# Kernel optimization log

Measured on AMD Instinct MI355X. Metric: run time of the kernel, lower is better.

Reference implementation:

```python
import jax, jax.numpy as jnp
import numpy as np

B, N_PER, F_IN, H1, EMB, N_ACT = 8, 50000, 64, 128, 64, 64
E_PER = 50000
N = B * N_PER  # flat node count


def setup_inputs() -> dict:
    key = jax.random.key(0)
    ks = jax.random.split(key, 6)
    s = lambda d: 1.0 / np.sqrt(d)
    return {
        "node_features": jax.random.normal(ks[0], (B, N_PER, F_IN), jnp.float32),
        "edge_index": jax.random.randint(ks[1], (B, 2, E_PER), 0, N, jnp.int64),
        "W1": jax.random.normal(ks[2], (F_IN, H1), jnp.float32) * s(F_IN),
        "b1": jnp.zeros((H1,), jnp.float32),
        "W2": jax.random.normal(ks[3], (H1, EMB), jnp.float32) * s(H1),
        "b2": jnp.zeros((EMB,), jnp.float32),
        "fc_w": jax.random.normal(ks[4], (EMB, EMB), jnp.float32) * s(EMB),
        "fc_b": jnp.zeros((EMB,), jnp.float32),
        "out_w": jax.random.normal(ks[5], (EMB, N_ACT), jnp.float32) * s(EMB),
        "out_b": jnp.zeros((N_ACT,), jnp.float32),
    }


def _gcn_conv(x, W, b, src, dst, n):
    # PyG GCNConv: add self-loops, symmetric deg normalization, then
    # out_i = sum_{j->i} norm_ji * (x_j @ W) + b
    loop = jnp.arange(n, dtype=src.dtype)
    s2 = jnp.concatenate([src, loop])
    d2 = jnp.concatenate([dst, loop])
    deg = jax.ops.segment_sum(jnp.ones_like(s2, dtype=x.dtype), d2, num_segments=n)
    dis = jnp.where(deg > 0, jax.lax.rsqrt(deg), 0.0)
    norm = dis[s2] * dis[d2]  # [E+N]
    h = x @ W  # [n, out]
    msg = h[s2] * norm[:, None]  # gather + scale
    return jax.ops.segment_sum(msg, d2, num_segments=n) + b


def reference(node_features, edge_index, W1, b1, W2, b2, fc_w, fc_b, out_w, out_b):
    b_, n_, f_ = node_features.shape
    x = node_features.reshape(-1, f_)  # [B*N, F]
    ei = edge_index.reshape(2, -1)     # matches torch .view(2, -1) on contiguous tensor
    src, dst = ei[0], ei[1]
    n = b_ * n_
    x = jax.nn.relu(_gcn_conv(x, W1, b1, src, dst, n))
    x = jax.nn.relu(_gcn_conv(x, W2, b2, src, dst, n))
    # global_mean_pool with batch = arange(B).repeat_interleave(N): nodes are contiguous
    pooled = x.reshape(b_, n_, -1).mean(axis=1)  # [B, EMB]
    h = jax.nn.relu(pooled @ fc_w + fc_b)
    return h @ out_w + out_b  # [B, num_actions]
```

## Files before the change

kernel.cpp:

```cpp
#include <hip/hip_runtime.h>

#define NPER 50000
#define NB 8
#define FIN 64
#define NH1 128
#define NEMB 64

typedef __attribute__((ext_vector_type(8))) short short8;
typedef __attribute__((ext_vector_type(4))) float f32x4;
union U4S8 { uint4 q; short8 s; };

__device__ inline float bf2f(unsigned int u){ union{unsigned int i; float f;} v; v.i = u<<16; return v.f; }
__device__ inline unsigned int f2bf1(float f){ union{float f; unsigned int i;} v; v.f = f;
  return (v.i + 0x7FFFu + ((v.i>>16)&1u)) >> 16; }
__device__ inline unsigned int packbf(float lo, float hi){ return f2bf1(lo) | (f2bf1(hi)<<16); }
__device__ inline void unp8add(float* s, uint4 q){
  s[0]+=bf2f(q.x&0xFFFFu); s[1]+=bf2f(q.x>>16);
  s[2]+=bf2f(q.y&0xFFFFu); s[3]+=bf2f(q.y>>16);
  s[4]+=bf2f(q.z&0xFFFFu); s[5]+=bf2f(q.z>>16);
  s[6]+=bf2f(q.w&0xFFFFu); s[7]+=bf2f(q.w>>16);
}

__global__ void k_detect(const int* __restrict__ ei, int* __restrict__ flag){
  __shared__ int any;
  if(threadIdx.x == 0) any = 0;
  __syncthreads();
  for(int i = threadIdx.x; i < 2048; i += 256){
    if(ei[2*i + 1] != 0) any = 1;
  }
  __syncthreads();
  if(threadIdx.x == 0) *flag = (any == 0) ? 1 : 0;
}
__device__ inline int load_edge(const int* __restrict__ ei, int idx, bool is64){
  return is64 ? ei[2*idx] : ei[idx];
}

__global__ void k_packW(const float* __restrict__ W1, const float* __restrict__ W2,
                        unsigned int* __restrict__ w1p, unsigned int* __restrict__ w2p){
  int tid = threadIdx.x;
  for(int s = tid; s < 1024; s += 256){
    int f = s >> 6, lane = s & 63;
    int nt = f >> 1, kb = f & 1, g = lane >> 4, c = nt*16 + (lane & 15);
    unsigned int o[4];
    #pragma unroll
    for(int j = 0; j < 4; j++){
      int k0 = kb*32 + g*8 + 2*j;
      o[j] = packbf(W1[k0*NH1 + c], W1[(k0+1)*NH1 + c]);
    }
    *(uint4*)(w1p + s*4) = make_uint4(o[0],o[1],o[2],o[3]);
  }
  for(int s = tid; s < 1024; s += 256){
    int f = s >> 6, lane = s & 63;
    int nt = f >> 2, kb = f & 3, g = lane >> 4, c = nt*16 + (lane & 15);
    unsigned int o[4];
    #pragma unroll
    for(int j = 0; j < 4; j++){
      int k0 = kb*32 + g*8 + 2*j;
      o[j] = packbf(W2[k0*NEMB + c], W2[(k0+1)*NEMB + c]);
    }
    *(uint4*)(w2p + s*4) = make_uint4(o[0],o[1],o[2],o[3]);
  }
}

__global__ void k_count(const int* __restrict__ ei, const int* __restrict__ flag,
                        int* __restrict__ ideg, int E){
  int e = blockIdx.x*256 + threadIdx.x;
  if(e < E){
    bool is64 = (*flag != 0);
    int d = load_edge(ei, E + e, is64);
    atomicAdd(&ideg[d], 1);
  }
}

__global__ void k_scan1(const int* __restrict__ ideg, int* __restrict__ bsum, int n){
  __shared__ int red[256];
  int i0 = blockIdx.x*1024 + threadIdx.x*4;
  int t = 0;
  #pragma unroll
  for(int j = 0; j < 4; j++) if(i0+j < n) t += ideg[i0+j];
  red[threadIdx.x] = t;
  __syncthreads();
  for(int off = 128; off > 0; off >>= 1){
    if(threadIdx.x < off) red[threadIdx.x] += red[threadIdx.x + off];
    __syncthreads();
  }
  if(threadIdx.x == 0) bsum[blockIdx.x] = red[0];
}

__global__ void k_scan2(int* __restrict__ bsum, int* __restrict__ row_start, int nblk, int n){
  __shared__ int sm[512];
  int t = threadIdx.x;
  int v = (t < nblk) ? bsum[t] : 0;
  sm[t] = v;
  __syncthreads();
  for(int off = 1; off < 512; off <<= 1){
    int a = (t >= off) ? sm[t - off] : 0;
    __syncthreads();
    sm[t] += a;
    __syncthreads();
  }
  if(t < nblk) bsum[t] = sm[t] - v;
  if(t == 511) row_start[n] = sm[511];
}

__global__ void k_scan3(const int* __restrict__ ideg, const int* __restrict__ bsum,
                        int* __restrict__ row_start, int* __restrict__ cursor, int n){
  __shared__ int red[256];
  int i0 = blockIdx.x*1024 + threadIdx.x*4;
  int v[4]; int t = 0;
  #pragma unroll
  for(int j = 0; j < 4; j++){ v[j] = (i0+j < n) ? ideg[i0+j] : 0; t += v[j]; }
  red[threadIdx.x] = t;
  __syncthreads();
  for(int off = 1; off < 256; off <<= 1){
    int a = (threadIdx.x >= off) ? red[threadIdx.x - off] : 0;
    __syncthreads();
    red[threadIdx.x] += a;
    __syncthreads();
  }
  int run = bsum[blockIdx.x] + red[threadIdx.x] - t;
  #pragma unroll
  for(int j = 0; j < 4; j++){
    if(i0+j < n){ row_start[i0+j] = run; cursor[i0+j] = run; run += v[j]; }
  }
}

__global__ void k_dis(const int* __restrict__ ideg, float* __restrict__ dis, int n){
  int i = blockIdx.x*256 + threadIdx.x;
  if(i < n) dis[i] = rsqrtf((float)ideg[i] + 1.0f);
}

__global__ void k_fill(const int* __restrict__ ei, const int* __restrict__ flag,
                       int* __restrict__ cursor, int* __restrict__ src_list, int E){
  int e = blockIdx.x*256 + threadIdx.x;
  if(e < E){
    bool is64 = (*flag != 0);
    int s = load_edge(ei, e, is64);
    int d = load_edge(ei, E + e, is64);
    int pos = atomicAdd(&cursor[d], 1);
    src_list[pos] = s;
  }
}

__global__ __launch_bounds__(256) void k_gemm1m(const float* __restrict__ x, const unsigned int* __restrict__ w1p,
                                                const float* __restrict__ dis, unsigned int* __restrict__ g1, int n){
  __shared__ unsigned short tile[4][2176];
  const int tid = threadIdx.x;
  const int wm = tid >> 6, lane = tid & 63;
  const int m16 = lane & 15, g = lane >> 4;
  const int base = blockIdx.x*64;
  const int nodeA = base + wm*16 + m16;
  short8 a[2];
  #pragma unroll
  for(int kb = 0; kb < 2; kb++){
    float4 v0, v1;
    if(nodeA < n){
      const float* xp = x + (size_t)nodeA*FIN + kb*32 + g*8;
      v0 = *(const float4*)xp; v1 = *(const float4*)(xp + 4);
    } else { v0 = make_float4(0,0,0,0); v1 = v0; }
    U4S8 u;
    u.q.x = packbf(v0.x, v0.y); u.q.y = packbf(v0.z, v0.w);
    u.q.z = packbf(v1.x, v1.y); u.q.w = packbf(v1.z, v1.w);
    a[kb] = u.s;
  }
  f32x4 acc[8] = {};
  #pragma unroll
  for(int nt = 0; nt < 8; nt++){
    #pragma unroll
    for(int kb = 0; kb < 2; kb++){
      U4S8 b; b.q = *(const uint4*)(w1p + ((nt*2 + kb)*64 + lane)*4);
      acc[nt] = __builtin_amdgcn_mfma_f32_16x16x32_bf16(a[kb], b.s, acc[nt], 0, 0, 0);
    }
  }
  float dr[4];
  #pragma unroll
  for(int i = 0; i < 4; i++){ int r = base + wm*16 + 4*g + i; dr[i] = (r < n) ? dis[r] : 0.f; }
  unsigned short* T = tile[wm];
  #pragma unroll
  for(int nt = 0; nt < 8; nt++)
    #pragma unroll
    for(int i = 0; i < 4; i++)
      T[(4*g + i)*136 + nt*16 + m16] = (unsigned short)f2bf1(acc[nt][i] * dr[i]);
  __syncthreads();
  int r = lane >> 2;
  int node2 = base + wm*16 + r;
  if(node2 < n){
    uint4* dst = (uint4*)(g1 + (size_t)node2*64);
    #pragma unroll
    for(int j = 0; j < 4; j++){
      int q = (lane & 3)*4 + j;
      dst[q] = *(const uint4*)(T + r*136 + q*8);
    }
  }
}

__global__ __launch_bounds__(256) void k_fused1m(const unsigned int* __restrict__ g1, const unsigned int* __restrict__ w2p,
                                                 const float* __restrict__ dis, const float* __restrict__ b1,
                                                 const int* __restrict__ row_start, const int* __restrict__ src_list,
                                                 unsigned int* __restrict__ g2, int n){
  __shared__ unsigned int x1T[4352];
  const int tid = threadIdx.x;
  const int base = blockIdx.x*64;
  {
    int nl = tid >> 2, qc = tid & 3;
    int node = base + nl;
    int rbase = nl*68 + qc*16;
    int sw = (nl & 7) << 2;
    if(node < n){
      float s[32];
      #pragma unroll
      for(int j = 0; j < 32; j++) s[j] = 0.f;
      const uint4* self = (const uint4*)(g1 + (size_t)node*64 + qc*16);
      { uint4 q0 = self[0], q1 = self[1], q2 = self[2], q3 = self[3];
        unp8add(s, q0); unp8add(s+8, q1); unp8add(s+16, q2); unp8add(s+24, q3); }
      int r0 = row_start[node], r1 = row_start[node+1];
      for(int e = r0; e < r1; e++){
        const uint4* p = (const uint4*)(g1 + (size_t)src_list[e]*64 + qc*16);
        uint4 q0 = p[0], q1 = p[1], q2 = p[2], q3 = p[3];
        unp8add(s, q0); unp8add(s+8, q1); unp8add(s+16, q2); unp8add(s+24, q3);
      }
      float d = dis[node];
      const float* bb = b1 + qc*32;
      unsigned int ob[16];
      #pragma unroll
      for(int j = 0; j < 16; j++){
        float v0 = fmaxf(fmaf(d, s[2*j],   bb[2*j]),   0.f);
        float v1 = fmaxf(fmaf(d, s[2*j+1], bb[2*j+1]), 0.f);
        ob[j] = packbf(v0, v1);
      }
      #pragma unroll
      for(int j = 0; j < 4; j++)
        *(uint4*)(x1T + ((rbase + j*4) ^ sw)) = make_uint4(ob[4*j], ob[4*j+1], ob[4*j+2], ob[4*j+3]);
    } else {
      #pragma unroll
      for(int j = 0; j < 4; j++)
        *(uint4*)(x1T + ((rbase + j*4) ^ sw)) = make_uint4(0,0,0,0);
    }
  }
  __syncthreads();
  const int wm = tid >> 6, lane = tid & 63, m16 = lane & 15, g = lane >> 4;
  const int row = wm*16 + m16;
  const int swr = (row & 7) << 2;
  f32x4 acc[4] = {};
  #pragma unroll
  for(int kb = 0; kb < 4; kb++){
    U4S8 a; a.q = *(const uint4*)(x1T + ((row*68 + kb*16 + g*4) ^ swr));
    #pragma unroll
    for(int nt = 0; nt < 4; nt++){
      U4S8 b; b.q = *(const uint4*)(w2p + ((nt*4 + kb)*64 + lane)*4);
      acc[nt] = __builtin_amdgcn_mfma_f32_16x16x32_bf16(a.s, b.s, acc[nt], 0, 0, 0);
    }
  }
  __syncthreads();
  unsigned short* T = (unsigned short*)x1T + wm*1152;
  float dr[4];
  #pragma unroll
  for(int i = 0; i < 4; i++){ int r = base + wm*16 + 4*g + i; dr[i] = (r < n) ? dis[r] : 0.f; }
  #pragma unroll
  for(int nt = 0; nt < 4; nt++)
    #pragma unroll
    for(int i = 0; i < 4; i++)
      T[(4*g + i)*72 + nt*16 + m16] = (unsigned short)f2bf1(acc[nt][i] * dr[i]);
  __syncthreads();
  int r = lane >> 2;
  int node2 = base + wm*16 + r;
  if(node2 < n){
    uint4* dst = (uint4*)(g2 + (size_t)node2*32);
    #pragma unroll
    for(int j = 0; j < 2; j++){
      int q = ((lane & 3) << 1) + j;
      dst[q] = *(const uint4*)(T + r*72 + q*8);
    }
  }
}

__global__ __launch_bounds__(256) void k_fused2p(const unsigned int* __restrict__ g2,
                                                 const float* __restrict__ dis, const float* __restrict__ b2,
                                                 const int* __restrict__ row_start, const int* __restrict__ src_list,
                                                 float* __restrict__ pooled, int n){
  __shared__ float red[256*17];
  const int tid = threadIdx.x;
  const int base = blockIdx.x*64;
  int nl = tid >> 2, qc = tid & 3;
  int node = base + nl;
  float s[16];
  #pragma unroll
  for(int j = 0; j < 16; j++) s[j] = 0.f;
  if(node < n){
    const uint4* self = (const uint4*)(g2 + (size_t)node*32 + qc*8);
    { uint4 q0 = self[0], q1 = self[1]; unp8add(s, q0); unp8add(s+8, q1); }
    int r0 = row_start[node], r1 = row_start[node+1];
    for(int e = r0; e < r1; e++){
      const uint4* p = (const uint4*)(g2 + (size_t)src_list[e]*32 + qc*8);
      uint4 q0 = p[0], q1 = p[1];
      unp8add(s, q0); unp8add(s+8, q1);
    }
    float d = dis[node];
    const float* bb = b2 + qc*16;
    #pragma unroll
    for(int j = 0; j < 16; j++) s[j] = fmaxf(fmaf(d, s[j], bb[j]), 0.f);
  }
  #pragma unroll
  for(int j = 0; j < 16; j++) red[tid*17 + j] = s[j];
  __syncthreads();
  if(tid < 64){
    int qc2 = tid >> 4, c = tid & 15;
    int b0 = base / NPER;
    int split = (b0 + 1)*NPER - base;
    float s0 = 0.f, s1 = 0.f;
    for(int m = 0; m < 64; m++){
      float v = red[(m*4 + qc2)*17 + c];
      if(m < split) s0 += v; else s1 += v;
    }
    unsafeAtomicAdd(&pooled[b0*64 + qc2*16 + c], s0);
    if(split < 64 && b0 + 1 < NB) unsafeAtomicAdd(&pooled[(b0+1)*64 + qc2*16 + c], s1);
  }
}

__global__ void k_head(const float* __restrict__ pooled, const float* __restrict__ fcw,
                       const float* __restrict__ fcb, const float* __restrict__ ow,
                       const float* __restrict__ ob, float* __restrict__ out){
  __shared__ float p[NB*NEMB];
  __shared__ float h[NB*NEMB];
  int t = threadIdx.x;
  p[t] = pooled[t] * (1.0f / (float)NPER);
  __syncthreads();
  int b = t >> 6, j = t & 63;
  float a = fcb[j];
  #pragma unroll 8
  for(int c = 0; c < 64; c++) a = fmaf(p[b*64+c], fcw[c*64+j], a);
  h[t] = fmaxf(a, 0.f);
  __syncthreads();
  float o = ob[j];
  #pragma unroll 8
  for(int c = 0; c < 64; c++) o = fmaf(h[b*64+c], ow[c*64+j], o);
  out[t] = o;
}

extern "C" void kernel_launch(void* const* d_in, const int* in_sizes, int n_in,
                              void* d_out, int out_size, void* d_ws, size_t ws_size,
                              hipStream_t stream){
  const float* x   = (const float*)d_in[0];
  const int*   ei  = (const int*)d_in[1];
  const float* W1  = (const float*)d_in[2];
  const float* b1  = (const float*)d_in[3];
  const float* W2  = (const float*)d_in[4];
  const float* b2  = (const float*)d_in[5];
  const float* fcw = (const float*)d_in[6];
  const float* fcb = (const float*)d_in[7];
  const float* ow  = (const float*)d_in[8];
  const float* ob  = (const float*)d_in[9];

  const int n = in_sizes[0] / FIN;
  const int E = in_sizes[1] / 2;

  char* p = (char*)d_ws;
  auto alloc = [&](size_t bytes){ char* r = p; p += (bytes + 255) & ~(size_t)255; return r; };
  float* dis      = (float*)alloc((size_t)n*4);
  int*   ideg     = (int*)  alloc((size_t)n*4);
  int*   row_start= (int*)  alloc((size_t)(n+1)*4);
  int*   cursor   = (int*)  alloc((size_t)n*4);
  int*   bsum     = (int*)  alloc(4096);
  int*   flag     = (int*)  alloc(256);
  float* pooled   = (float*)alloc(2048);
  unsigned int* w1p = (unsigned int*)alloc(16384);
  unsigned int* w2p = (unsigned int*)alloc(16384);
  int*   src_list = (int*)  alloc((size_t)E*4);
  unsigned int* g1 = (unsigned int*)alloc((size_t)n*64*4);
  unsigned int* g2 = (unsigned int*)alloc((size_t)n*32*4);

  hipMemsetAsync(ideg, 0, (size_t)n*4, stream);
  hipMemsetAsync(pooled, 0, 2048, stream);

  k_detect<<<1, 256, 0, stream>>>(ei, flag);
  k_packW<<<1, 256, 0, stream>>>(W1, W2, w1p, w2p);
  k_count<<<(E+255)/256, 256, 0, stream>>>(ei, flag, ideg, E);
  int nblk = (n + 1023)/1024;
  k_scan1<<<nblk, 256, 0, stream>>>(ideg, bsum, n);
  k_scan2<<<1, 512, 0, stream>>>(bsum, row_start, nblk, n);
  k_scan3<<<nblk, 256, 0, stream>>>(ideg, bsum, row_start, cursor, n);
  k_dis<<<(n+255)/256, 256, 0, stream>>>(ideg, dis, n);
  k_fill<<<(E+255)/256, 256, 0, stream>>>(ei, flag, cursor, src_list, E);

  k_gemm1m<<<(n+63)/64, 256, 0, stream>>>(x, w1p, dis, g1, n);
  k_fused1m<<<(n+63)/64, 256, 0, stream>>>(g1, w2p, dis, b1, row_start, src_list, g2, n);
  k_fused2p<<<(n+63)/64, 256, 0, stream>>>(g2, dis, b2, row_start, src_list, pooled, n);

  k_head<<<1, 512, 0, stream>>>(pooled, fcw, fcb, ow, ob, (float*)d_out);
}
```

Measured before the change: 392.3 us.

## Aggregate raw inputs before first GEMM and fuse both GCN layers' matmuls

Reorders layer one to aggregate normalized 64-wide fp32 input features over neighbours first, then apply W1. This lets a single kernel do aggregation, the W1 GEMM with bias and ReLU, and the W2 GEMM, and it removes the 128-wide bf16 g1 intermediate and its gather traffic. Gathering fp32 x rows (256 B) plus a per-edge dis lookup replaces gathering 256 B bf16 g1 rows. It also merges the detect, packW and memset steps into one init kernel, and folds the dis computation into scan3, cutting launches.

```diff
diff --git a/kernel.cpp b/kernel.cpp
--- a/kernel.cpp
+++ b/kernel.cpp
@@ -20,45 +20,53 @@
   s[4]+=bf2f(q.z&0xFFFFu); s[5]+=bf2f(q.z>>16);
   s[6]+=bf2f(q.w&0xFFFFu); s[7]+=bf2f(q.w>>16);
 }
-
-__global__ void k_detect(const int* __restrict__ ei, int* __restrict__ flag){
-  __shared__ int any;
-  if(threadIdx.x == 0) any = 0;
-  __syncthreads();
-  for(int i = threadIdx.x; i < 2048; i += 256){
-    if(ei[2*i + 1] != 0) any = 1;
-  }
-  __syncthreads();
-  if(threadIdx.x == 0) *flag = (any == 0) ? 1 : 0;
-}
 __device__ inline int load_edge(const int* __restrict__ ei, int idx, bool is64){
   return is64 ? ei[2*idx] : ei[idx];
 }
 
-__global__ void k_packW(const float* __restrict__ W1, const float* __restrict__ W2,
-                        unsigned int* __restrict__ w1p, unsigned int* __restrict__ w2p){
-  int tid = threadIdx.x;
-  for(int s = tid; s < 1024; s += 256){
-    int f = s >> 6, lane = s & 63;
-    int nt = f >> 1, kb = f & 1, g = lane >> 4, c = nt*16 + (lane & 15);
-    unsigned int o[4];
+__global__ void k_init(const int* __restrict__ ei, const float* __restrict__ W1, const float* __restrict__ W2,
+                       int* __restrict__ flag, unsigned int* __restrict__ w1p, unsigned int* __restrict__ w2p,
+                       int* __restrict__ ideg, float* __restrict__ pooled, int n){
+  const int b = blockIdx.x, tid = threadIdx.x;
+  if(b == 0){
+    __shared__ int any;
+    if(tid == 0) any = 0;
+    __syncthreads();
+    for(int i = tid; i < 2048; i += 256) if(ei[2*i + 1] != 0) any = 1;
+    __syncthreads();
+    if(tid == 0) *flag = (any == 0) ? 1 : 0;
+    if(tid < 256){ pooled[tid] = 0.f; pooled[tid + 256] = 0.f; }
+  } else if(b == 1){
+    for(int s = tid; s < 1024; s += 256){
+      int f = s >> 6, lane = s & 63;
+      int nt = f >> 1, kb = f & 1, g = lane >> 4, c = nt*16 + (lane & 15);
+      unsigned int o[4];
+      #pragma unroll
+      for(int j = 0; j < 4; j++){
+        int k0 = kb*32 + g*8 + 2*j;
+        o[j] = packbf(W1[k0*NH1 + c], W1[(k0+1)*NH1 + c]);
+      }
+      *(uint4*)(w1p + s*4) = make_uint4(o[0],o[1],o[2],o[3]);
+    }
+    for(int s = tid; s < 1024; s += 256){
+      int f = s >> 6, lane = s & 63;
+      int nt = f >> 2, kb = f & 3, g = lane >> 4, c = nt*16 + (lane & 15);
+      unsigned int o[4];
+      #pragma unroll
+      for(int j = 0; j < 4; j++){
+        int k0 = kb*32 + g*8 + 2*j;
+        o[j] = packbf(W2[k0*NEMB + c], W2[(k0+1)*NEMB + c]);
+      }
+      *(uint4*)(w2p + s*4) = make_uint4(o[0],o[1],o[2],o[3]);
+    }
+  } else {
+    int i0 = (b-2)*4096 + tid*16;
     #pragma unroll
     for(int j = 0; j < 4; j++){
-      int k0 = kb*32 + g*8 + 2*j;
-      o[j] = packbf(W1[k0*NH1 + c], W1[(k0+1)*NH1 + c]);
-    }
-    *(uint4*)(w1p + s*4) = make_uint4(o[0],o[1],o[2],o[3]);
-  }
-  for(int s = tid; s < 1024; s += 256){
-    int f = s >> 6, lane = s & 63;
-    int nt = f >> 2, kb = f & 3, g = lane >> 4, c = nt*16 + (lane & 15);
-    unsigned int o[4];
-    #pragma unroll
-    for(int j = 0; j < 4; j++){
-      int k0 = kb*32 + g*8 + 2*j;
-      o[j] = packbf(W2[k0*NEMB + c], W2[(k0+1)*NEMB + c]);
-    }
-    *(uint4*)(w2p + s*4) = make_uint4(o[0],o[1],o[2],o[3]);
+      int i = i0 + j*4;
+      if(i + 3 < n) *(int4*)(ideg + i) = make_int4(0,0,0,0);
+      else for(int k = 0; k < 4; k++) if(i + k < n) ideg[i+k] = 0;
+    }
   }
 }
 
@@ -104,7 +112,8 @@
 }
 
 __global__ void k_scan3(const int* __restrict__ ideg, const int* __restrict__ bsum,
-                        int* __restrict__ row_start, int* __restrict__ cursor, int n){
+                        int* __restrict__ row_start, int* __restrict__ cursor,
+                        float* __restrict__ dis, int n){
   __shared__ int red[256];
   int i0 = blockIdx.x*1024 + threadIdx.x*4;
   int v[4]; int t = 0;
@@ -121,13 +130,11 @@
   int run = bsum[blockIdx.x] + red[threadIdx.x] - t;
   #pragma unroll
   for(int j = 0; j < 4; j++){
-    if(i0+j < n){ row_start[i0+j] = run; cursor[i0+j] = run; run += v[j]; }
-  }
-}
-
-__global__ void k_dis(const int* __restrict__ ideg, float* __restrict__ dis, int n){
-  int i = blockIdx.x*256 + threadIdx.x;
-  if(i < n) dis[i] = rsqrtf((float)ideg[i] + 1.0f);
+    if(i0+j < n){
+      row_start[i0+j] = run; cursor[i0+j] = run; run += v[j];
+      dis[i0+j] = rsqrtf((float)v[j] + 1.0f);
+    }
+  }
 }
 
 __global__ void k_fill(const int* __restrict__ ei, const int* __restrict__ flag,
@@ -142,142 +149,132 @@
   }
 }
 
-__global__ __launch_bounds__(256) void k_gemm1m(const float* __restrict__ x, const unsigned int* __restrict__ w1p,
-                                                const float* __restrict__ dis, unsigned int* __restrict__ g1, int n){
-  __shared__ unsigned short tile[4][2176];
-  const int tid = threadIdx.x;
-  const int wm = tid >> 6, lane = tid & 63;
-  const int m16 = lane & 15, g = lane >> 4;
-  const int base = blockIdx.x*64;
-  const int nodeA = base + wm*16 + m16;
-  short8 a[2];
-  #pragma unroll
-  for(int kb = 0; kb < 2; kb++){
-    float4 v0, v1;
-    if(nodeA < n){
-      const float* xp = x + (size_t)nodeA*FIN + kb*32 + g*8;
-      v0 = *(const float4*)xp; v1 = *(const float4*)(xp + 4);
-    } else { v0 = make_float4(0,0,0,0); v1 = v0; }
-    U4S8 u;
-    u.q.x = packbf(v0.x, v0.y); u.q.y = packbf(v0.z, v0.w);
-    u.q.z = packbf(v1.x, v1.y); u.q.w = packbf(v1.z, v1.w);
-    a[kb] = u.s;
-  }
-  f32x4 acc[8] = {};
-  #pragma unroll
-  for(int nt = 0; nt < 8; nt++){
-    #pragma unroll
-    for(int kb = 0; kb < 2; kb++){
-      U4S8 b; b.q = *(const uint4*)(w1p + ((nt*2 + kb)*64 + lane)*4);
-      acc[nt] = __builtin_amdgcn_mfma_f32_16x16x32_bf16(a[kb], b.s, acc[nt], 0, 0, 0);
-    }
-  }
-  float dr[4];
-  #pragma unroll
-  for(int i = 0; i < 4; i++){ int r = base + wm*16 + 4*g + i; dr[i] = (r < n) ? dis[r] : 0.f; }
-  unsigned short* T = tile[wm];
-  #pragma unroll
-  for(int nt = 0; nt < 8; nt++)
-    #pragma unroll
-    for(int i = 0; i < 4; i++)
-      T[(4*g + i)*136 + nt*16 + m16] = (unsigned short)f2bf1(acc[nt][i] * dr[i]);
-  __syncthreads();
-  int r = lane >> 2;
-  int node2 = base + wm*16 + r;
-  if(node2 < n){
-    uint4* dst = (uint4*)(g1 + (size_t)node2*64);
-    #pragma unroll
-    for(int j = 0; j < 4; j++){
-      int q = (lane & 3)*4 + j;
-      dst[q] = *(const uint4*)(T + r*136 + q*8);
-    }
-  }
-}
-
-__global__ __launch_bounds__(256) void k_fused1m(const unsigned int* __restrict__ g1, const unsigned int* __restrict__ w2p,
-                                                 const float* __restrict__ dis, const float* __restrict__ b1,
-                                                 const int* __restrict__ row_start, const int* __restrict__ src_list,
-                                                 unsigned int* __restrict__ g2, int n){
-  __shared__ unsigned int x1T[4352];
+__global__ __launch_bounds__(256) void k_A(const float* __restrict__ x,
+                                           const unsigned int* __restrict__ w1p, const unsigned int* __restrict__ w2p,
+                                           const float* __restrict__ dis, const float* __restrict__ b1,
+                                           const int* __restrict__ row_start, const int* __restrict__ src_list,
+                                           unsigned int* __restrict__ g2, int n){
+  __shared__ unsigned int aggT[64*36];
+  __shared__ unsigned int x1t[4][16*68];
+  __shared__ float sb1[NH1];
   const int tid = threadIdx.x;
   const int base = blockIdx.x*64;
-  {
-    int nl = tid >> 2, qc = tid & 3;
-    int node = base + nl;
-    int rbase = nl*68 + qc*16;
-    int sw = (nl & 7) << 2;
+
+  if(tid < NH1) sb1[tid] = b1[tid];
+  {
+    const int nl = tid >> 2, qc = tid & 3;
+    const int node = base + nl;
+    const int sw = (nl & 7) << 2;
+    unsigned int* dst = aggT + nl*36;
     if(node < n){
-      float s[32];
-      #pragma unroll
-      for(int j = 0; j < 32; j++) s[j] = 0.f;
-      const uint4* self = (const uint4*)(g1 + (size_t)node*64 + qc*16);
-      { uint4 q0 = self[0], q1 = self[1], q2 = self[2], q3 = self[3];
-        unp8add(s, q0); unp8add(s+8, q1); unp8add(s+16, q2); unp8add(s+24, q3); }
+      float dn = dis[node];
+      float s[16];
+      {
+        const float4* xp = (const float4*)(x + (size_t)node*FIN + qc*16);
+        float4 v0 = xp[0], v1 = xp[1], v2 = xp[2], v3 = xp[3];
+        s[0]=dn*v0.x; s[1]=dn*v0.y; s[2]=dn*v0.z; s[3]=dn*v0.w;
+        s[4]=dn*v1.x; s[5]=dn*v1.y; s[6]=dn*v1.z; s[7]=dn*v1.w;
+        s[8]=dn*v2.x; s[9]=dn*v2.y; s[10]=dn*v2.z; s[11]=dn*v2.w;
+        s[12]=dn*v3.x; s[13]=dn*v3.y; s[14]=dn*v3.z; s[15]=dn*v3.w;
+      }
       int r0 = row_start[node], r1 = row_start[node+1];
       for(int e = r0; e < r1; e++){
-        const uint4* p = (const uint4*)(g1 + (size_t)src_list[e]*64 + qc*16);
-        uint4 q0 = p[0], q1 = p[1], q2 = p[2], q3 = p[3];
-        unp8add(s, q0); unp8add(s+8, q1); unp8add(s+16, q2); unp8add(s+24, q3);
-      }
-      float d = dis[node];
-      const float* bb = b1 + qc*32;
-      unsigned int ob[16];
-      #pragma unroll
-      for(int j = 0; j < 16; j++){
-        float v0 = fmaxf(fmaf(d, s[2*j],   bb[2*j]),   0.f);
-        float v1 = fmaxf(fmaf(d, s[2*j+1], bb[2*j+1]), 0.f);
-        ob[j] = packbf(v0, v1);
-      }
-      #pragma unroll
-      for(int j = 0; j < 4; j++)
-        *(uint4*)(x1T + ((rbase + j*4) ^ sw)) = make_uint4(ob[4*j], ob[4*j+1], ob[4*j+2], ob[4*j+3]);
+        int src = src_list[e];
+        float ds = dis[src];
+        const float4* p = (const float4*)(x + (size_t)src*FIN + qc*16);
+        float4 v0 = p[0], v1 = p[1], v2 = p[2], v3 = p[3];
+        s[0]=fmaf(ds,v0.x,s[0]); s[1]=fmaf(ds,v0.y,s[1]); s[2]=fmaf(ds,v0.z,s[2]); s[3]=fmaf(ds,v0.w,s[3]);
+        s[4]=fmaf(ds,v1.x,s[4]); s[5]=fmaf(ds,v1.y,s[5]); s[6]=fmaf(ds,v1.z,s[6]); s[7]=fmaf(ds,v1.w,s[7]);
+        s[8]=fmaf(ds,v2.x,s[8]); s[9]=fmaf(ds,v2.y,s[9]); s[10]=fmaf(ds,v2.z,s[10]); s[11]=fmaf(ds,v2.w,s[11]);
+        s[12]=fmaf(ds,v3.x,s[12]); s[13]=fmaf(ds,v3.y,s[13]); s[14]=fmaf(ds,v3.z,s[14]); s[15]=fmaf(ds,v3.w,s[15]);
+      }
+      unsigned int ob[8];
+      #pragma unroll
+      for(int j = 0; j < 8; j++) ob[j] = packbf(s[2*j]*dn, s[2*j+1]*dn);
+      *(uint4*)(dst + ((qc*8    ) ^ sw)) = make_uint4(ob[0],ob[1],ob[2],ob[3]);
+      *(uint4*)(dst + ((qc*8 + 4) ^ sw)) = make_uint4(ob[4],ob[5],ob[6],ob[7]);
     } else {
-      #pragma unroll
-      for(int j = 0; j < 4; j++)
-        *(uint4*)(x1T + ((rbase + j*4) ^ sw)) = make_uint4(0,0,0,0);
-    }
-  }
-  __syncthreads();
+      *(uint4*)(dst + ((qc*8    ) ^ sw)) = make_uint4(0,0,0,0);
+      *(uint4*)(dst + ((qc*8 + 4) ^ sw)) = make_uint4(0,0,0,0);
+    }
+  }
+  __syncthreads();
+
   const int wm = tid >> 6, lane = tid & 63, m16 = lane & 15, g = lane >> 4;
-  const int row = wm*16 + m16;
-  const int swr = (row & 7) << 2;
-  f32x4 acc[4] = {};
-  #pragma unroll
-  for(int kb = 0; kb < 4; kb++){
-    U4S8 a; a.q = *(const uint4*)(x1T + ((row*68 + kb*16 + g*4) ^ swr));
-    #pragma unroll
-    for(int nt = 0; nt < 4; nt++){
-      U4S8 b; b.q = *(const uint4*)(w2p + ((nt*4 + kb)*64 + lane)*4);
-      acc[nt] = __builtin_amdgcn_mfma_f32_16x16x32_bf16(a.s, b.s, acc[nt], 0, 0, 0);
-    }
-  }
-  __syncthreads();
-  unsigned short* T = (unsigned short*)x1T + wm*1152;
-  float dr[4];
-  #pragma unroll
-  for(int i = 0; i < 4; i++){ int r = base + wm*16 + 4*g + i; dr[i] = (r < n) ? dis[r] : 0.f; }
-  #pragma unroll
-  for(int nt = 0; nt < 4; nt++)
-    #pragma unroll
-    for(int i = 0; i < 4; i++)
-      T[(4*g + i)*72 + nt*16 + m16] = (unsigned short)f2bf1(acc[nt][i] * dr[i]);
-  __syncthreads();
-  int r = lane >> 2;
-  int node2 = base + wm*16 + r;
-  if(node2 < n){
-    uint4* dst = (uint4*)(g2 + (size_t)node2*32);
-    #pragma unroll
-    for(int j = 0; j < 2; j++){
-      int q = ((lane & 3) << 1) + j;
-      dst[q] = *(const uint4*)(T + r*72 + q*8);
-    }
-  }
-}
-
-__global__ __launch_bounds__(256) void k_fused2p(const unsigned int* __restrict__ g2,
-                                                 const float* __restrict__ dis, const float* __restrict__ b2,
-                                                 const int* __restrict__ row_start, const int* __restrict__ src_list,
-                                                 float* __restrict__ pooled, int n){
+  {
+    const int row = wm*16 + m16;
+    const int swr = (row & 7) << 2;
+    f32x4 acc[8] = {};
+    #pragma unroll
+    for(int kb = 0; kb < 2; kb++){
+      U4S8 a; a.q = *(const uint4*)(aggT + row*36 + ((kb*16 + g*4) ^ swr));
+      #pragma unroll
+      for(int nt = 0; nt < 8; nt++){
+        U4S8 b; b.q = *(const uint4*)(w1p + ((nt*2 + kb)*64 + lane)*4);
+        acc[nt] = __builtin_amdgcn_mfma_f32_16x16x32_bf16(a.s, b.s, acc[nt], 0, 0, 0);
+      }
+    }
+    unsigned short* T = (unsigned short*)x1t[wm];
+    #pragma unroll
+    for(int i = 0; i < 4; i++){
+      int r = 4*g + i;
+      int swx = (r & 7) << 2;
+      #pragma unroll
+      for(int nt = 0; nt < 8; nt++){
+        int c = nt*16 + m16;
+        float v = fmaxf(acc[nt][i] + sb1[c], 0.f);
+        T[r*136 + 2*(((c >> 1) ^ swx)) + (c & 1)] = (unsigned short)f2bf1(v);
+      }
+    }
+  }
+  __syncthreads();
+
+  f32x4 acc2[4] = {};
+  {
+    const int swr = (m16 & 7) << 2;
+    #pragma unroll
+    for(int kb = 0; kb < 4; kb++){
+      U4S8 a; a.q = *(const uint4*)(x1t[wm] + m16*68 + ((kb*16 + g*4) ^ swr));
+      #pragma unroll
+      for(int nt = 0; nt < 4; nt++){
+        U4S8 b; b.q = *(const uint4*)(w2p + ((nt*4 + kb)*64 + lane)*4);
+        acc2[nt] = __builtin_amdgcn_mfma_f32_16x16x32_bf16(a.s, b.s, acc2[nt], 0, 0, 0);
+      }
+    }
+  }
+  __syncthreads();
+
+  {
+    unsigned short* T = (unsigned short*)aggT + wm*1152;
+    float dr[4];
+    #pragma unroll
+    for(int i = 0; i < 4; i++){ int r = base + wm*16 + 4*g + i; dr[i] = (r < n) ? dis[r] : 0.f; }
+    #pragma unroll
+    for(int nt = 0; nt < 4; nt++)
+      #pragma unroll
+      for(int i = 0; i < 4; i++)
+        T[(4*g + i)*72 + nt*16 + m16] = (unsigned short)f2bf1(acc2[nt][i] * dr[i]);
+  }
+  __syncthreads();
+  {
+    unsigned short* T = (unsigned short*)aggT + wm*1152;
+    int r = lane >> 2;
+    int node2 = base + wm*16 + r;
+    if(node2 < n){
+      uint4* dst = (uint4*)(g2 + (size_t)node2*32);
+      #pragma unroll
+      for(int j = 0; j < 2; j++){
+        int q = ((lane & 3) << 1) + j;
+        dst[q] = *(const uint4*)(T + r*72 + q*8);
+      }
+    }
+  }
+}
+
+__global__ __launch_bounds__(256) void k_B(const unsigned int* __restrict__ g2,
+                                           const float* __restrict__ dis, const float* __restrict__ b2,
+                                           const int* __restrict__ row_start, const int* __restrict__ src_list,
+                                           float* __restrict__ pooled, int n){
   __shared__ float red[256*17];
   const int tid = threadIdx.x;
   const int base = blockIdx.x*64;
@@ -366,25 +363,18 @@
   unsigned int* w1p = (unsigned int*)alloc(16384);
   unsigned int* w2p = (unsigned int*)alloc(16384);
   int*   src_list = (int*)  alloc((size_t)E*4);
-  unsigned int* g1 = (unsigned int*)alloc((size_t)n*64*4);
   unsigned int* g2 = (unsigned int*)alloc((size_t)n*32*4);
 
-  hipMemsetAsync(ideg, 0, (size_t)n*4, stream);
-  hipMemsetAsync(pooled, 0, 2048, stream);
-
-  k_detect<<<1, 256, 0, stream>>>(ei, flag);
-  k_packW<<<1, 256, 0, stream>>>(W1, W2, w1p, w2p);
+  int zblk = (n + 4095)/4096;
+  k_init<<<2 + zblk, 256, 0, stream>>>(ei, W1, W2, flag, w1p, w2p, ideg, pooled, n);
   k_count<<<(E+255)/256, 256, 0, stream>>>(ei, flag, ideg, E);
   int nblk = (n + 1023)/1024;
   k_scan1<<<nblk, 256, 0, stream>>>(ideg, bsum, n);
   k_scan2<<<1, 512, 0, stream>>>(bsum, row_start, nblk, n);
-  k_scan3<<<nblk, 256, 0, stream>>>(ideg, bsum, row_start, cursor, n);
-  k_dis<<<(n+255)/256, 256, 0, stream>>>(ideg, dis, n);
+  k_scan3<<<nblk, 256, 0, stream>>>(ideg, bsum, row_start, cursor, dis, n);
   k_fill<<<(E+255)/256, 256, 0, stream>>>(ei, flag, cursor, src_list, E);
 
-  k_gemm1m<<<(n+63)/64, 256, 0, stream>>>(x, w1p, dis, g1, n);
-  k_fused1m<<<(n+63)/64, 256, 0, stream>>>(g1, w2p, dis, b1, row_start, src_list, g2, n);
-  k_fused2p<<<(n+63)/64, 256, 0, stream>>>(g2, dis, b2, row_start, src_list, pooled, n);
-
+  k_A<<<(n+63)/64, 256, 0, stream>>>(x, w1p, w2p, dis, b1, row_start, src_list, g2, n);
+  k_B<<<(n+63)/64, 256, 0, stream>>>(g2, dis, b2, row_start, src_list, pooled, n);
   k_head<<<1, 512, 0, stream>>>(pooled, fcw, fcb, ow, ob, (float*)d_out);
 }
```

New measurement: 344.2 us. 1.14x faster.
